# Kernel optimization log

Measured on AMD Instinct MI355X. Metric: run time of the kernel, lower is better.

## Reference

```python
import jax, jax.numpy as jnp
import numpy as np

EMBED_DIM = 256
NUM_HEADS = 8
HEAD_DIM = EMBED_DIM // NUM_HEADS
SCALING = HEAD_DIM ** -0.5
SEQ = 1024
BSZ = 4


def setup_inputs() -> dict:
    rng = jax.random.key(0)
    ks = jax.random.split(rng, 5)
    E = EMBED_DIM
    q = jax.random.normal(ks[0], (SEQ, BSZ, E), jnp.float32)
    k = jax.random.normal(ks[1], (SEQ, BSZ, E), jnp.float32)
    v = jax.random.normal(ks[2], (SEQ, BSZ, E), jnp.float32)
    # xavier-uniform-like scale for the packed 9E x E projection
    lim_in = np.sqrt(6.0 / (9 * E + E)).astype(np.float32)
    in_proj_w = jax.random.uniform(ks[3], (9 * E, E), jnp.float32, -lim_in, lim_in)
    in_proj_b = jnp.zeros((9 * E,), jnp.float32)
    lim_out = np.sqrt(6.0 / (E + E)).astype(np.float32)
    out_w = jax.random.uniform(ks[4], (E, E), jnp.float32, -lim_out, lim_out)
    out_b = jnp.zeros((E,), jnp.float32)
    return {"query": q, "key": k, "value": v,
            "in_proj_w": in_proj_w, "in_proj_b": in_proj_b,
            "out_w": out_w, "out_b": out_b,
            "shape0": 32, "shape1": 32}


def reference(query, key, value, in_proj_w, in_proj_b, out_w, out_b, shape0, shape1):
    S, B, E = query.shape
    H, hd = NUM_HEADS, HEAD_DIM

    def proj(x, i):  # slice i of the packed in-projection
        return x @ in_proj_w[i * E:(i + 1) * E].T + in_proj_b[i * E:(i + 1) * E]

    def heads(x):  # [S,B,E] -> [B*H, S, hd]
        return x.reshape(S, B * H, hd).transpose(1, 0, 2)

    q      = heads(proj(query, 0) * SCALING)
    k      = heads(proj(key, 1))
    v      = heads(proj(value, 2))
    q_left = heads(proj(query, 3))
    k_left = heads(proj(key, 4))
    q_right = heads(proj(query, 5))
    k_right = heads(proj(key, 6))
    q_loc  = heads(proj(query, 7) * SCALING)
    k_loc  = heads(proj(key, 8))

    global_w = q @ k.transpose(0, 2, 1)        # [BH,S,S]
    local_w  = q_loc @ k_loc.transpose(0, 2, 1)

    left_sm  = jax.nn.softmax(q_left @ k_left.transpose(0, 2, 1), axis=-1)
    right_sm = jax.nn.softmax(q_right @ k_right.transpose(0, 2, 1), axis=-1)

    triu = jnp.triu(jnp.ones((S, S), query.dtype))
    mini = jnp.tile(jnp.triu(jnp.ones((shape1, shape1), query.dtype)), (shape0, shape0))
    triu = (triu * mini)[None]                 # [1,S,S]
    triu_t = triu.transpose(0, 2, 1)

    fw_mask = (left_sm @ triu) * (right_sm @ triu_t)
    bw_mask = (left_sm @ triu_t) * (right_sm @ triu)
    local_mask = fw_mask + bw_mask             # [BH,S,S]

    attn_w = jax.nn.softmax(0.1 * global_w + local_w * local_mask, axis=-1)
    attn = (attn_w @ v).transpose(1, 0, 2).reshape(S, B, E)
    attn = attn @ out_w.T + out_b
    consistent_mask = local_mask.sum(axis=0)   # [S,S]
    return attn, consistent_mask
```

## Files before the change

kernel.cpp:

```cpp
#include <hip/hip_runtime.h>


typedef _Float16 v8h __attribute__((ext_vector_type(8)));
typedef _Float16 v4h __attribute__((ext_vector_type(4)));
typedef _Float16 v2h __attribute__((ext_vector_type(2)));
typedef float    v4f __attribute__((ext_vector_type(4)));

#define SL 1048576
#define RS 1032

static constexpr float SCALE = 0.17677669529663687f;


__global__ __launch_bounds__(256)
void cvt_kernel(const float* __restrict__ q, const float* __restrict__ k,
                const float* __restrict__ v, const float* __restrict__ W,
                _Float16* __restrict__ X16, _Float16* __restrict__ W16)
{
    const int b = blockIdx.x;
    const int t = threadIdx.x;
    const float* src; _Float16* dst; int off;
    if (b < 512)       { src = q; dst = X16;             off = b; }
    else if (b < 1024) { src = k; dst = X16 + (1 << 20); off = b - 512; }
    else if (b < 1536) { src = v; dst = X16 + (2 << 20); off = b - 1024; }
    else               { src = W; dst = W16;             off = b - 1536; }
    const int i = off * 2048 + t * 8;
    const float4 a = *(const float4*)(src + i);
    const float4 c = *(const float4*)(src + i + 4);
    v8h h;
    h[0] = (_Float16)a.x; h[1] = (_Float16)a.y; h[2] = (_Float16)a.z; h[3] = (_Float16)a.w;
    h[4] = (_Float16)c.x; h[5] = (_Float16)c.y; h[6] = (_Float16)c.z; h[7] = (_Float16)c.w;
    *(v8h*)(dst + i) = h;
}

__global__ __launch_bounds__(256)
void proj_kernel(const _Float16* __restrict__ X16, const _Float16* __restrict__ W16,
                 const float* __restrict__ bias, _Float16* __restrict__ P)
{
    __shared__ __align__(16) _Float16 stage[4096];
    const int t  = threadIdx.x;
    const int n0 = blockIdx.x * 64;
    const int m0 = blockIdx.y * 64;
    const int slice = n0 >> 8;
    const int q2 = (n0 >> 6) & 3;
    const bool kslice = (slice == 1) || (slice == 4) || (slice == 6) || (slice == 8);
    const _Float16* X = X16 + (slice == 2 ? (2 << 20) : (kslice ? (1 << 20) : 0));
    const int w = t >> 6, lane = t & 63, m16 = lane & 15, kg = lane >> 4;
    const v4f zero = {0.f, 0.f, 0.f, 0.f};
    v4f acc[4] = {zero, zero, zero, zero};
    const _Float16* Arow = X + (size_t)(m0 + w * 16 + m16) * 256 + kg * 8;
    const _Float16* B0   = W16 + (size_t)(n0 + m16) * 256 + kg * 8;
#pragma unroll
    for (int kk = 0; kk < 8; ++kk) {
        const v8h a = *(const v8h*)(Arow + kk * 32);
#pragma unroll
        for (int nf = 0; nf < 4; ++nf) {
            const v8h bb = *(const v8h*)(B0 + nf * 4096 + kk * 32);
            acc[nf] = __builtin_amdgcn_mfma_f32_16x16x32_f16(a, bb, acc[nf], 0, 0, 0);
        }
    }
    const float scale = (slice == 0 || slice == 7) ? SCALE : 1.0f;
#pragma unroll
    for (int nf = 0; nf < 4; ++nf) {
        const int c = n0 + nf * 16 + m16;
        const float bv = bias[c];
#pragma unroll
        for (int i = 0; i < 4; ++i) {
            const _Float16 val = (_Float16)((acc[nf][i] + bv) * scale);
            const int lb = i * 2 + (nf >> 1);
            int inner;
            if (slice == 2) {
                const int ls = w * 4 + kg;
                inner = ((nf & 1) << 8) + ((ls >> 3) << 7) + m16 * 8 + (ls & 7);
            } else {
                inner = ((w * 4 + kg) + (((nf & 1) * 2 + (m16 >> 3)) << 4)) * 8 + (m16 & 7);
            }
            stage[lb * 512 + inner] = val;
        }
    }
    __syncthreads();
    {
        const int o  = t * 16;
        const int lb = o >> 9;
        const int inner = o & 511;
        const int bs = lb >> 1, hh = lb & 1;
        const int bh = bs * 8 + 2 * q2 + hh;
        size_t dst;
        if (slice == 2) {
            const int kc = m0 >> 7;
            const int g0 = (m0 >> 5) & 3;
            const int nt = inner >> 8, a = (inner >> 7) & 1, r = inner & 127;
            dst = (size_t)2 * SL + (size_t)bh * 32768
                + (size_t)(kc * 1024 + nt * 512 + (g0 + a) * 128 + r);
        } else {
            const int tile = m0 >> 6;
            dst = (size_t)slice * SL + (size_t)bh * 32768 + (size_t)(tile * 512 + inner);
        }
        *(v8h*)(P + dst)     = *(const v8h*)(stage + o);
        *(v8h*)(P + dst + 8) = *(const v8h*)(stage + o + 8);
    }
}

__global__ __launch_bounds__(512, 4)
void attn_kernel(const _Float16* __restrict__ P, float* __restrict__ attn_pre,
                 _Float16* __restrict__ pmask)
{
    __shared__ __align__(16) _Float16 Lh[16 * RS];
    __shared__ __align__(16) _Float16 Rh[16 * RS];

    const int t    = threadIdx.x;
    const int bid  = blockIdx.x;
    const int q    = bid >> 3;
    const int bh   = ((bid & 7) << 2) + (q & 3);
    const int rt   = q >> 2;
    const int w    = __builtin_amdgcn_readfirstlane(t >> 6);
    const int lane = t & 63;
    const int m16  = lane & 15;
    const int kg   = lane >> 4;

    const _Float16* Pb = P + (size_t)bh * 32768;
    const v4f zero = {0.f, 0.f, 0.f, 0.f};

    {
        const v8h a_l = *(const v8h*)(Pb + 3 * SL + rt * 512 + lane * 8);
        const v8h a_r = *(const v8h*)(Pb + 5 * SL + rt * 512 + lane * 8);
        const _Float16* Bl = Pb + 4 * SL;
        const _Float16* Br = Pb + 6 * SL;
#pragma unroll 4
        for (int jt2 = 0; jt2 < 8; ++jt2) {
            const int jt = (w << 3) + jt2;
            const v8h bL = *(const v8h*)(Bl + jt * 512 + lane * 8);
            const v8h bR = *(const v8h*)(Br + jt * 512 + lane * 8);
            v4f cL = __builtin_amdgcn_mfma_f32_16x16x32_f16(a_l, bL, zero, 0, 0, 0);
            v4f cR = __builtin_amdgcn_mfma_f32_16x16x32_f16(a_r, bR, zero, 0, 0, 0);
            const int col = (jt << 4) + m16;
#pragma unroll
            for (int i = 0; i < 4; ++i) {
                Lh[((kg << 2) + i) * RS + col] = (_Float16)cL[i];
                Rh[((kg << 2) + i) * RS + col] = (_Float16)cR[i];
            }
        }
    }
    __syncthreads();

    {
        const int kr = lane & 31;
        for (int r = 0; r < 2; ++r) {
            _Float16* ROW = (lane >= 32) ? &Rh[((w << 1) + r) * RS] : &Lh[((w << 1) + r) * RS];
            float x[32];
#pragma unroll
            for (int kb = 0; kb < 32; ++kb)
                x[kb] = __expf((float)ROW[(kb << 5) + kr]);
#pragma unroll
            for (int kb = 0; kb < 32; ++kb) {
#pragma unroll
                for (int off = 1; off < 32; off <<= 1) {
                    const float y = __shfl_up(x[kb], off, 32);
                    if (kr >= off) x[kb] += y;
                }
            }
#pragma unroll
            for (int kb = 1; kb < 32; ++kb) x[kb] += x[kb - 1];
            const float inv = 1.f / __shfl(x[31], 31, 32);
#pragma unroll
            for (int kb = 0; kb < 32; ++kb)
                ROW[(kb << 5) + kr] = (_Float16)(x[kb] * inv);
        }
    }
    __syncthreads();

    v4h sc4[8];
    {
        _Float16* pm = pmask + (size_t)bh * 1048576 + (size_t)rt * 16384;
        const v8h a_g = *(const v8h*)(Pb + 0 * SL + rt * 512 + lane * 8);
        const v8h a_c = *(const v8h*)(Pb + 7 * SL + rt * 512 + lane * 8);
        const _Float16* Bg = Pb + 1 * SL;
        const _Float16* Bc = Pb + 8 * SL;
#pragma unroll
        for (int jt2 = 0; jt2 < 8; ++jt2) {
            const int jt  = (w << 3) + jt2;
            const int jb  = jt >> 1;
            const int jr  = ((jt & 1) << 4) + m16;
            const int col = (jt << 4) + m16;
            const v8h bG = *(const v8h*)(Bg + jt * 512 + lane * 8);
            const v8h bC = *(const v8h*)(Bc + jt * 512 + lane * 8);
            const v4f g4 = __builtin_amdgcn_mfma_f32_16x16x32_f16(a_g, bG, zero, 0, 0, 0);
            const v4f l4 = __builtin_amdgcn_mfma_f32_16x16x32_f16(a_c, bC, zero, 0, 0, 0);
            v4h s4, m4;
#pragma unroll
            for (int i = 0; i < 4; ++i) {
                const int rr = ((kg << 2) + i) * RS;
                const float PL  = (float)Lh[rr + col];
                const float PR  = (float)Rh[rr + col];
                const float eLb = jb ? (float)Lh[rr + (jb << 5) - 1] : 0.f;
                const float eRb = jb ? (float)Rh[rr + (jb << 5) - 1] : 0.f;
                const float eLc = jr ? (float)Lh[rr + 991 + jr] : 0.f;
                const float eRc = jr ? (float)Rh[rr + 991 + jr] : 0.f;
                const float eLbc = (jb && jr) ? (float)Lh[rr + ((jb - 1) << 5) + jr - 1] : 0.f;
                const float eRbc = (jb && jr) ? (float)Rh[rr + ((jb - 1) << 5) + jr - 1] : 0.f;
                const float SLv = 1.0f - eLb - eLc + eLbc;
                const float SRv = 1.0f - eRb - eRc + eRbc;
                const float mkv = PL * SRv + SLv * PR;
                s4[i] = (_Float16)(0.1f * g4[i] + l4[i] * mkv);
                m4[i] = (_Float16)mkv;
            }
            sc4[jt2] = s4;
            *(v4h*)(pm + ((size_t)jt << 8) + (lane << 2)) = m4;
        }
    }
    __syncthreads();

    {
#pragma unroll
        for (int jt2 = 0; jt2 < 8; ++jt2) {
            const int col = ((((w << 3) + jt2)) << 4) + m16;
#pragma unroll
            for (int i = 0; i < 4; ++i)
                Lh[((kg << 2) + i) * RS + col] = sc4[jt2][i];
        }
    }
    __syncthreads();

    auto softmax_pairs = [&](_Float16* ROW) {
        float v0[8], v1[8];
        float ss = 0.f;
#pragma unroll
        for (int kq = 0; kq < 8; ++kq) {
            const v2h pr = *(const v2h*)&ROW[(lane + (kq << 6)) << 1];
            v0[kq] = __expf((float)pr[0]);
            v1[kq] = __expf((float)pr[1]);
            ss += v0[kq] + v1[kq];
        }
#pragma unroll
        for (int off = 32; off; off >>= 1) ss += __shfl_xor(ss, off);
        const float inv = 1.f / ss;
#pragma unroll
        for (int kq = 0; kq < 8; ++kq) {
            v2h pr; pr[0] = (_Float16)(v0[kq] * inv); pr[1] = (_Float16)(v1[kq] * inv);
            *(v2h*)&ROW[(lane + (kq << 6)) << 1] = pr;
        }
    };
#pragma unroll
    for (int r = 0; r < 2; ++r) softmax_pairs(&Lh[((w << 1) + r) * RS]);
    __syncthreads();

    {
        const int nt = w & 1, hf = w >> 1;
        v4f c = zero;
        const _Float16* Vb = Pb + 2 * SL + nt * 512 + lane * 8;
        const int kc0 = hf << 3;
#pragma unroll 4
        for (int kc2 = 0; kc2 < 8; ++kc2) {
            const int kc = kc0 + kc2;
            const v8h a = *(const v8h*)&Lh[m16 * RS + (kc << 5) + (kg << 3)];
            const v8h b = *(const v8h*)(Vb + (size_t)kc * 1024);
            c = __builtin_amdgcn_mfma_f32_16x16x32_f16(a, b, c, 0, 0, 0);
        }
        float* Pbuf = (float*)&Rh[0];
#pragma unroll
        for (int i = 0; i < 4; ++i) Pbuf[(w << 8) + (lane << 2) + i] = c[i];
    }
    __syncthreads();

    {
        const float* Pbuf = (const float*)&Rh[0];
        const int r   = t >> 5;
        const int d   = t & 31;
        const int nt2 = d >> 4, n = d & 15;
        const int kg2 = r >> 2, i2 = r & 3;
        const int off = (kg2 << 6) + (n << 2) + i2;
        float v = 0.f;
#pragma unroll
        for (int hf = 0; hf < 4; ++hf)
            v += Pbuf[(((hf << 1) + nt2) << 8) + off];
        const int srow = (rt << 4) + r;
        attn_pre[((size_t)(srow * 4 + (bh >> 3))) * 256 + (bh & 7) * 32 + d] = v;
    }
}

__global__ __launch_bounds__(256)
void tail_kernel(const _Float16* __restrict__ pmask, float* __restrict__ cmask,
                 const float* __restrict__ A, const float* __restrict__ W,
                 const float* __restrict__ bias, float* __restrict__ C)
{
    __shared__ __align__(16) float SMEM[4 * 16 * 132];
    const int bid = blockIdx.x;
    const int t = threadIdx.x;

    if (bid >= 256) {
        const int b2 = bid - 256;
        const int rt = b2 >> 3, wh = b2 & 7;
        float (*T4)[16][132] = (float(*)[16][132])SMEM;
        const int wv = t >> 6;
        const int lane = t & 63, m16 = lane & 15, kg = lane >> 4;
        float acc[8][4] = {};
        const _Float16* base = pmask + (size_t)rt * 16384 + ((size_t)wh << 11) + (lane << 2)
                             + ((size_t)wv << 3) * 1048576;
        for (int bh = 0; bh < 8; ++bh) {
            const _Float16* p = base + (size_t)bh * 1048576;
#pragma unroll
            for (int jt2 = 0; jt2 < 8; ++jt2) {
                const v4h h4 = *(const v4h*)(p + (jt2 << 8));
#pragma unroll
                for (int i = 0; i < 4; ++i) acc[jt2][i] += (float)h4[i];
            }
        }
#pragma unroll
        for (int jt2 = 0; jt2 < 8; ++jt2)
#pragma unroll
            for (int i = 0; i < 4; ++i)
                T4[wv][(kg << 2) + i][(jt2 << 4) + m16] = acc[jt2][i];
        __syncthreads();
        const int row = t >> 4;
        const int c0  = (t & 15) << 3;
#pragma unroll
        for (int h = 0; h < 2; ++h) {
            const int c = c0 + (h << 2);
            const float4 s0 = *(const float4*)&T4[0][row][c];
            const float4 s1 = *(const float4*)&T4[1][row][c];
            const float4 s2 = *(const float4*)&T4[2][row][c];
            const float4 s3 = *(const float4*)&T4[3][row][c];
            const float4 o = make_float4(s0.x + s1.x + s2.x + s3.x,
                                         s0.y + s1.y + s2.y + s3.y,
                                         s0.z + s1.z + s2.z + s3.z,
                                         s0.w + s1.w + s2.w + s3.w);
            *(float4*)&cmask[((size_t)((rt << 4) + row) << 10) + (wh << 7) + c] = o;
        }
    } else {
        const int n0 = (bid & 3) * 64;
        const int m0 = (bid >> 2) * 64;
        float (*As)[68] = (float(*)[68])SMEM;
        float (*Bs)[68] = (float(*)[68])(SMEM + 16 * 68);
        const int tx = t & 15, ty = t >> 4;
        const int lm = t >> 2, lk = (t & 3) << 2;
        float acc[4][4] = {};
        for (int k0 = 0; k0 < 256; k0 += 16) {
            float4 av = *(const float4*)(A + (size_t)(m0 + lm) * 256 + k0 + lk);
            float4 bv = *(const float4*)(W + (size_t)(n0 + lm) * 256 + k0 + lk);
            As[lk + 0][lm] = av.x; As[lk + 1][lm] = av.y; As[lk + 2][lm] = av.z; As[lk + 3][lm] = av.w;
            Bs[lk + 0][lm] = bv.x; Bs[lk + 1][lm] = bv.y; Bs[lk + 2][lm] = bv.z; Bs[lk + 3][lm] = bv.w;
            __syncthreads();
#pragma unroll
            for (int kk = 0; kk < 16; ++kk) {
                float4 a4 = *(const float4*)&As[kk][ty << 2];
                float4 b4 = *(const float4*)&Bs[kk][tx << 2];
                float aa[4] = {a4.x, a4.y, a4.z, a4.w};
                float bb[4] = {b4.x, b4.y, b4.z, b4.w};
#pragma unroll
                for (int i = 0; i < 4; ++i)
#pragma unroll
                    for (int j = 0; j < 4; ++j)
                        acc[i][j] = fmaf(aa[i], bb[j], acc[i][j]);
            }
            __syncthreads();
        }
#pragma unroll
        for (int i = 0; i < 4; ++i) {
            const int m  = m0 + (ty << 2) + i;
            const int c0 = n0 + (tx << 2);
            float4 o = make_float4(acc[i][0] + bias[c0 + 0], acc[i][1] + bias[c0 + 1],
                                   acc[i][2] + bias[c0 + 2], acc[i][3] + bias[c0 + 3]);
            *(float4*)&C[(size_t)m * 256 + c0] = o;
        }
    }
}

extern "C" void kernel_launch(void* const* d_in, const int* in_sizes, int n_in,
                              void* d_out, int out_size, void* d_ws, size_t ws_size,
                              hipStream_t stream)
{
    const float* q  = (const float*)d_in[0];
    const float* k  = (const float*)d_in[1];
    const float* v  = (const float*)d_in[2];
    const float* Wi = (const float*)d_in[3];
    const float* bi = (const float*)d_in[4];
    const float* Wo = (const float*)d_in[5];
    const float* bo = (const float*)d_in[6];

    float* out      = (float*)d_out;
    float* attn_out = out;
    float* cmask    = out + 1048576;

    _Float16* Ppack    = (_Float16*)d_ws;
    float*    attn_pre = (float*)((char*)d_ws + 18874368);
    _Float16* pmask    = (_Float16*)((char*)d_ws + 23068672);
    _Float16* X16      = (_Float16*)((char*)d_ws + 90177536);
    _Float16* W16      = (_Float16*)((char*)d_ws + 96468992);

    cvt_kernel<<<1824, 256, 0, stream>>>(q, k, v, Wi, X16, W16);
    proj_kernel<<<dim3(36, 64), 256, 0, stream>>>(X16, W16, bi, Ppack);
    attn_kernel<<<2048, 512, 0, stream>>>(Ppack, attn_pre, pmask);
    tail_kernel<<<768, 256, 0, stream>>>(pmask, cmask, attn_pre, Wo, bo, attn_out);
}
```

Baseline: 276.7 us.

## Transpose MFMA operands for vectorized LDS stores and cache prefix-sum edges

Swaps the A/B operands of the MFMA calls so each lane holds four consecutive columns of a row. The Lh/Rh score tiles, the pmask tile and the score buffer can then be written and read with 4-wide half vector accesses instead of scalar strided ones. The last-block cumulative values are stored in small edge arrays during the scan, which removes several scattered LDS loads per element in the mask-construction step. The pmask tile layout changes to match, and the tail reduction's shared-memory indexing and padding are updated to fit it.

```diff
diff --git a/kernel.cpp b/kernel.cpp
--- a/kernel.cpp
+++ b/kernel.cpp
@@ -107,6 +107,8 @@
 {
     __shared__ __align__(16) _Float16 Lh[16 * RS];
     __shared__ __align__(16) _Float16 Rh[16 * RS];
+    __shared__ __align__(16) _Float16 Ledge[16][36];
+    __shared__ __align__(16) _Float16 Redge[16][36];
 
     const int t    = threadIdx.x;
     const int bid  = blockIdx.x;
@@ -131,14 +133,14 @@
             const int jt = (w << 3) + jt2;
             const v8h bL = *(const v8h*)(Bl + jt * 512 + lane * 8);
             const v8h bR = *(const v8h*)(Br + jt * 512 + lane * 8);
-            v4f cL = __builtin_amdgcn_mfma_f32_16x16x32_f16(a_l, bL, zero, 0, 0, 0);
-            v4f cR = __builtin_amdgcn_mfma_f32_16x16x32_f16(a_r, bR, zero, 0, 0, 0);
-            const int col = (jt << 4) + m16;
-#pragma unroll
-            for (int i = 0; i < 4; ++i) {
-                Lh[((kg << 2) + i) * RS + col] = (_Float16)cL[i];
-                Rh[((kg << 2) + i) * RS + col] = (_Float16)cR[i];
-            }
+            v4f cL = __builtin_amdgcn_mfma_f32_16x16x32_f16(bL, a_l, zero, 0, 0, 0);
+            v4f cR = __builtin_amdgcn_mfma_f32_16x16x32_f16(bR, a_r, zero, 0, 0, 0);
+            v4h hL, hR;
+#pragma unroll
+            for (int i = 0; i < 4; ++i) { hL[i] = (_Float16)cL[i]; hR[i] = (_Float16)cR[i]; }
+            const int base = m16 * RS + (jt << 4) + (kg << 2);
+            *(v4h*)&Lh[base] = hL;
+            *(v4h*)&Rh[base] = hR;
         }
     }
     __syncthreads();
@@ -146,7 +148,8 @@
     {
         const int kr = lane & 31;
         for (int r = 0; r < 2; ++r) {
-            _Float16* ROW = (lane >= 32) ? &Rh[((w << 1) + r) * RS] : &Lh[((w << 1) + r) * RS];
+            const int row = (w << 1) + r;
+            _Float16* ROW = (lane >= 32) ? &Rh[row * RS] : &Lh[row * RS];
             float x[32];
 #pragma unroll
             for (int kb = 0; kb < 32; ++kb)
@@ -162,6 +165,9 @@
 #pragma unroll
             for (int kb = 1; kb < 32; ++kb) x[kb] += x[kb - 1];
             const float inv = 1.f / __shfl(x[31], 31, 32);
+            _Float16* EG = (lane >= 32) ? &Redge[row][0] : &Ledge[row][0];
+            EG[kr + 1] = (_Float16)(x[31] * inv);
+            if (kr == 0) EG[0] = (_Float16)0.f;
 #pragma unroll
             for (int kb = 0; kb < 32; ++kb)
                 ROW[(kb << 5) + kr] = (_Float16)(x[kb] * inv);
@@ -176,28 +182,40 @@
         const v8h a_c = *(const v8h*)(Pb + 7 * SL + rt * 512 + lane * 8);
         const _Float16* Bg = Pb + 1 * SL;
         const _Float16* Bc = Pb + 8 * SL;
+        const int rr = m16 * RS;
 #pragma unroll
         for (int jt2 = 0; jt2 < 8; ++jt2) {
-            const int jt  = (w << 3) + jt2;
-            const int jb  = jt >> 1;
-            const int jr  = ((jt & 1) << 4) + m16;
-            const int col = (jt << 4) + m16;
+            const int jt   = (w << 3) + jt2;
+            const int jb   = jt >> 1;
+            const int jr0  = ((jt & 1) << 4) + (kg << 2);
+            const int colb = (jt << 4) + (kg << 2);
             const v8h bG = *(const v8h*)(Bg + jt * 512 + lane * 8);
             const v8h bC = *(const v8h*)(Bc + jt * 512 + lane * 8);
-            const v4f g4 = __builtin_amdgcn_mfma_f32_16x16x32_f16(a_g, bG, zero, 0, 0, 0);
-            const v4f l4 = __builtin_amdgcn_mfma_f32_16x16x32_f16(a_c, bC, zero, 0, 0, 0);
+            const v4f g4 = __builtin_amdgcn_mfma_f32_16x16x32_f16(bG, a_g, zero, 0, 0, 0);
+            const v4f l4 = __builtin_amdgcn_mfma_f32_16x16x32_f16(bC, a_c, zero, 0, 0, 0);
+            const v4h PLv  = *(const v4h*)&Lh[rr + colb];
+            const v4h PRv  = *(const v4h*)&Rh[rr + colb];
+            const v4h eLcv = *(const v4h*)&Ledge[m16][jr0];
+            const v4h eRcv = *(const v4h*)&Redge[m16][jr0];
+            float eLb = 0.f, eRb = 0.f;
+            if (jb) {
+                eLb = (float)Lh[rr + (jb << 5) - 1];
+                eRb = (float)Rh[rr + (jb << 5) - 1];
+            }
             v4h s4, m4;
 #pragma unroll
             for (int i = 0; i < 4; ++i) {
-                const int rr = ((kg << 2) + i) * RS;
-                const float PL  = (float)Lh[rr + col];
-                const float PR  = (float)Rh[rr + col];
-                const float eLb = jb ? (float)Lh[rr + (jb << 5) - 1] : 0.f;
-                const float eRb = jb ? (float)Rh[rr + (jb << 5) - 1] : 0.f;
-                const float eLc = jr ? (float)Lh[rr + 991 + jr] : 0.f;
-                const float eRc = jr ? (float)Rh[rr + 991 + jr] : 0.f;
-                const float eLbc = (jb && jr) ? (float)Lh[rr + ((jb - 1) << 5) + jr - 1] : 0.f;
-                const float eRbc = (jb && jr) ? (float)Rh[rr + ((jb - 1) << 5) + jr - 1] : 0.f;
+                const int jrv = jr0 + i;
+                const float PL  = (float)PLv[i];
+                const float PR  = (float)PRv[i];
+                const float eLc = (float)eLcv[i];
+                const float eRc = (float)eRcv[i];
+                float eLbc = 0.f, eRbc = 0.f;
+                if (jb && jrv) {
+                    const int o = rr + ((jb - 1) << 5) + jrv - 1;
+                    eLbc = (float)Lh[o];
+                    eRbc = (float)Rh[o];
+                }
                 const float SLv = 1.0f - eLb - eLc + eLbc;
                 const float SRv = 1.0f - eRb - eRc + eRbc;
                 const float mkv = PL * SRv + SLv * PR;
@@ -205,19 +223,15 @@
                 m4[i] = (_Float16)mkv;
             }
             sc4[jt2] = s4;
-            *(v4h*)(pm + ((size_t)jt << 8) + (lane << 2)) = m4;
-        }
-    }
-    __syncthreads();
-
-    {
-#pragma unroll
-        for (int jt2 = 0; jt2 < 8; ++jt2) {
-            const int col = ((((w << 3) + jt2)) << 4) + m16;
-#pragma unroll
-            for (int i = 0; i < 4; ++i)
-                Lh[((kg << 2) + i) * RS + col] = sc4[jt2][i];
-        }
+            *(v4h*)(pm + ((size_t)jt << 8) + (m16 << 4) + (kg << 2)) = m4;
+        }
+    }
+    __syncthreads();
+
+    {
+#pragma unroll
+        for (int jt2 = 0; jt2 < 8; ++jt2)
+            *(v4h*)&Lh[m16 * RS + (((w << 3) + jt2) << 4) + (kg << 2)] = sc4[jt2];
     }
     __syncthreads();
 
@@ -283,16 +297,16 @@
                  const float* __restrict__ A, const float* __restrict__ W,
                  const float* __restrict__ bias, float* __restrict__ C)
 {
-    __shared__ __align__(16) float SMEM[4 * 16 * 132];
+    __shared__ __align__(16) float SMEM[4 * 16 * 136];
     const int bid = blockIdx.x;
     const int t = threadIdx.x;
 
     if (bid >= 256) {
         const int b2 = bid - 256;
         const int rt = b2 >> 3, wh = b2 & 7;
-        float (*T4)[16][132] = (float(*)[16][132])SMEM;
+        float (*T4)[16][136] = (float(*)[16][136])SMEM;
         const int wv = t >> 6;
-        const int lane = t & 63, m16 = lane & 15, kg = lane >> 4;
+        const int lane = t & 63;
         float acc[8][4] = {};
         const _Float16* base = pmask + (size_t)rt * 16384 + ((size_t)wh << 11) + (lane << 2)
                              + ((size_t)wv << 3) * 1048576;
@@ -309,7 +323,7 @@
         for (int jt2 = 0; jt2 < 8; ++jt2)
 #pragma unroll
             for (int i = 0; i < 4; ++i)
-                T4[wv][(kg << 2) + i][(jt2 << 4) + m16] = acc[jt2][i];
+                T4[wv][lane >> 2][(jt2 << 4) + ((lane & 3) << 2) + i] = acc[jt2][i];
         __syncthreads();
         const int row = t >> 4;
         const int c0  = (t & 15) << 3;
```

New measurement: 260.7 us. -5.8%, faster.
